# Kernel optimization log

Hardware: AMD Instinct MI355X
Metric: run time of the kernel (lower is better)

## Reference

```python
import jax, jax.numpy as jnp
import numpy as np
from jax.scipy.special import gammaln

# dims
S, B, T, N = 8, 128, 256, 128      # samples, trials, time bins, neurons
L, Hh, Hd, Hl = 64, 128, 64, 128   # latent, backward-enc h, dynamics hidden, local-enc hidden


def kl_diag(m, P, mu, Q):
    # KL(N(m, diag P) || N(mu, diag Q)), summed over last dim
    return 0.5 * jnp.sum(jnp.log(Q) - jnp.log(P) + (P + (m - mu) ** 2) / Q - 1.0, axis=-1)


def setup_inputs() -> dict:
    key = jax.random.key(0)
    ks = jax.random.split(key, 12)
    g = lambda i, shape, s=0.1: s * jax.random.normal(ks[i], shape, dtype=jnp.float32)
    y = jax.random.randint(ks[0], (B, T, N), 0, 5).astype(jnp.float32)  # spike counts
    return dict(
        y=y, n_samples=S,
        W_be=g(1, (N, Hh)), b_be=jnp.zeros((Hh,), jnp.float32),
        W_ic=g(2, (Hh, 2 * L)), b_ic=jnp.zeros((2 * L,), jnp.float32),
        W_le1=g(3, (Hh + L, Hl)), b_le1=jnp.zeros((Hl,), jnp.float32),
        W_le2=g(4, (Hl, 2 * L)), b_le2=jnp.zeros((2 * L,), jnp.float32),
        W_dyn1=g(5, (L, Hd)), b_dyn1=jnp.zeros((Hd,), jnp.float32),
        W_dyn2=g(6, (Hd, L)), b_dyn2=jnp.zeros((L,), jnp.float32),
        C=g(7, (L, N)), b_c=jnp.full((N,), -1.0, jnp.float32),
        log_Q=jnp.full((L,), -2.0, jnp.float32),
        m_0=jnp.zeros((L,), jnp.float32),
        log_Q_0=jnp.zeros((L,), jnp.float32),
        eps0=jax.random.normal(ks[8], (S, B, L), dtype=jnp.float32),
        eps=jax.random.normal(ks[9], (T - 1, S, B, L), dtype=jnp.float32),
    )


def reference(y, n_samples, W_be, b_be, W_ic, b_ic, W_le1, b_le1, W_le2, b_le2,
              W_dyn1, b_dyn1, W_dyn2, b_dyn2, C, b_c, log_Q, m_0, log_Q_0, eps0, eps):
    Q = jax.nn.softplus(log_Q)
    Q0 = jax.nn.softplus(log_Q_0)

    # backward encoder: per-step MLP y -> h  [B,T,Hh]
    h = jnp.tanh(y @ W_be + b_be)

    # t = 0: init_c_encoder on h[:,0]
    mp0 = h[:, 0] @ W_ic + b_ic
    m0e, P0 = mp0[..., :L], jax.nn.softplus(mp0[..., L:])
    z0 = m0e + jnp.sqrt(P0) * eps0                       # [S,B,L]
    kl0 = kl_diag(m0e, P0, m_0, Q0)                      # [B]

    def mean_fn(z):
        return jnp.tanh(z @ W_dyn1 + b_dyn1) @ W_dyn2 + b_dyn2

    def step(z_prev, xs):
        h_t, eps_t = xs                                  # [B,Hh], [S,B,L]
        inp = jnp.concatenate(
            [jnp.broadcast_to(h_t, (n_samples,) + h_t.shape), z_prev], axis=-1)
        mp = jnp.tanh(inp @ W_le1 + b_le1) @ W_le2 + b_le2
        m_t, P_t = mp[..., :L], jax.nn.softplus(mp[..., L:])
        z_t = m_t + jnp.sqrt(P_t) * eps_t                # [S,B,L]
        kl_t = kl_diag(m_t, P_t, mean_fn(z_prev), Q).mean(axis=0)  # [B]
        return z_t, (z_t, kl_t)

    h_rest = jnp.swapaxes(h[:, 1:], 0, 1)                # [T-1,B,Hh]
    _, (z_rest, kl_rest) = jax.lax.scan(step, z0, (h_rest, eps))

    z = jnp.concatenate([z0[:, :, None], jnp.moveaxis(z_rest, 0, 2)], axis=2)  # [S,B,T,L]
    kl = jnp.concatenate([kl0[:, None], kl_rest.T], axis=1)                    # [B,T]

    # Poisson log-likelihood, summed over neurons, averaged over samples
    log_rate = z @ C + b_c                               # [S,B,T,N]
    ell = jnp.sum(y * log_rate - jnp.exp(log_rate) - gammaln(y + 1.0), axis=-1).mean(axis=0)  # [B,T]

    loss = (kl - ell).sum(axis=-1).mean()
    m_stat = z.mean(axis=0)                              # [B,T,L]
    return loss, z, m_stat
```

## Files before the change

kernel.cpp:

```cpp
#include <hip/hip_runtime.h>

constexpr int S = 8, B = 128, T = 256, N = 128;
constexpr int L = 64, Hh = 128, Hd = 64, Hl = 128;
constexpr int BT = B * T;

#define DEVFN __device__ __forceinline__

typedef float    f32x4_t __attribute__((ext_vector_type(4)));
typedef _Float16 f16x8_t __attribute__((ext_vector_type(8)));
typedef _Float16 f16x4_t __attribute__((ext_vector_type(4)));

DEVFN float softplus_f(float x) {
    return (x > 0.f) ? (x + log1pf(expf(-x))) : log1pf(expf(x));
}
DEVFN float softplus_fast(float x) {
    return fmaxf(x, 0.f) + __logf(1.f + __expf(-fabsf(x)));
}
DEVFN float fast_tanh(float x) {
    float ex = __builtin_exp2f(x * 2.885390081777927f);
    return 1.f - 2.f / (ex + 1.f);
}
DEVFN float gaOf(float yv) {
    int yi = (int)yv;
    return (yi < 2) ? 0.f
         : ((yi == 2) ? 0.6931471805599453f
         : ((yi == 3) ? 1.791759469228055f : 3.1780538303479458f));
}

__global__ __launch_bounds__(256) void kA(
        const float* __restrict__ y,
        const float* __restrict__ W_be, const float* __restrict__ b_be,
        const float* __restrict__ W_le1, const float* __restrict__ b_le1,
        float* __restrict__ A, float* __restrict__ h0) {
    __shared__ alignas(16) _Float16 yS[32][136];
    __shared__ alignas(16) _Float16 hS[32][152];
    __shared__ alignas(16) float    st[32][136];
    __shared__ float bbeS[128];

    const int tid = threadIdx.x;
    const int w = tid >> 6, l = tid & 63;
    const int lo = l & 15, hi = l >> 4;
    const int bt0 = blockIdx.x * 32;

    if (tid < 128) bbeS[tid] = b_be[tid];

    {
        const float4* y4 = (const float4*)(y + (size_t)bt0 * 128);
        #pragma unroll
        for (int k = 0; k < 4; ++k) {
            int i = k * 256 + tid;
            float4 v = y4[i];
            int row = i >> 5, c4 = (i & 31) * 4;
            f16x4_t h4;
            h4[0] = (_Float16)v.x; h4[1] = (_Float16)v.y;
            h4[2] = (_Float16)v.z; h4[3] = (_Float16)v.w;
            *(f16x4_t*)&yS[row][c4] = h4;
        }
    }

    f16x8_t awb[2][4], awa[2][4];
    #pragma unroll
    for (int ct = 0; ct < 2; ++ct)
        #pragma unroll
        for (int kt = 0; kt < 4; ++kt) {
            f16x8_t f, g;
            #pragma unroll
            for (int e = 0; e < 8; ++e) {
                size_t off = (size_t)(kt * 32 + 8 * hi + e) * 128 + (32 * w + 16 * ct + lo);
                f[e] = (_Float16)W_be[off];
                g[e] = (_Float16)W_le1[off];
            }
            awb[ct][kt] = f; awa[ct][kt] = g;
        }
    const f32x4_t bl0 = *(const f32x4_t*)&b_le1[32 * w + 4 * hi];
    const f32x4_t bl1 = *(const f32x4_t*)&b_le1[32 * w + 16 + 4 * hi];
    __syncthreads();

    #pragma unroll
    for (int rt = 0; rt < 2; ++rt) {
        f32x4_t acc0 = {0.f,0.f,0.f,0.f}, acc1 = {0.f,0.f,0.f,0.f};
        #pragma unroll
        for (int kt = 0; kt < 4; ++kt) {
            const f16x8_t bf = *(const f16x8_t*)&yS[16 * rt + lo][kt * 32 + 8 * hi];
            acc0 = __builtin_amdgcn_mfma_f32_16x16x32_f16(awb[0][kt], bf, acc0, 0, 0, 0);
            acc1 = __builtin_amdgcn_mfma_f32_16x16x32_f16(awb[1][kt], bf, acc1, 0, 0, 0);
        }
        *(f32x4_t*)&st[16 * rt + lo][32 * w + 4 * hi]      = acc0;
        *(f32x4_t*)&st[16 * rt + lo][32 * w + 16 + 4 * hi] = acc1;
    }
    __syncthreads();

    {
        const int trow = tid >> 3, cb = (tid & 7) * 16;
        const bool isH0 = ((bt0 & 255) == 0) && (trow == 0);
        float* h0p = h0 + (size_t)(bt0 >> 8) * 128;
        #pragma unroll
        for (int j = 0; j < 16; ++j) {
            float hv = fast_tanh(st[trow][cb + j] + bbeS[cb + j]);
            hS[trow][cb + j] = (_Float16)hv;
            if (isH0) h0p[cb + j] = hv;
        }
    }
    __syncthreads();

    #pragma unroll
    for (int rt = 0; rt < 2; ++rt) {
        f32x4_t acc0 = {0.f,0.f,0.f,0.f}, acc1 = {0.f,0.f,0.f,0.f};
        #pragma unroll
        for (int kt = 0; kt < 4; ++kt) {
            const f16x8_t bf = *(const f16x8_t*)&hS[16 * rt + lo][kt * 32 + 8 * hi];
            acc0 = __builtin_amdgcn_mfma_f32_16x16x32_f16(awa[0][kt], bf, acc0, 0, 0, 0);
            acc1 = __builtin_amdgcn_mfma_f32_16x16x32_f16(awa[1][kt], bf, acc1, 0, 0, 0);
        }
        acc0 += bl0; acc1 += bl1;
        float* Ar = A + (size_t)(bt0 + 16 * rt + lo) * 128;
        *(f32x4_t*)&Ar[32 * w + 4 * hi]      = acc0;
        *(f32x4_t*)&Ar[32 * w + 16 + 4 * hi] = acc1;
    }
}

__global__ __launch_bounds__(256) void kC(
        const float* __restrict__ Aglob,
        const float* __restrict__ W_le1, const float* __restrict__ W_le2,
        const float* __restrict__ b_le2,
        const float* __restrict__ W_dyn1, const float* __restrict__ b_dyn1,
        const float* __restrict__ W_dyn2, const float* __restrict__ b_dyn2,
        const float* __restrict__ log_Q, const float* __restrict__ eps,
        const float* __restrict__ h0g, const float* __restrict__ W_ic,
        const float* __restrict__ b_ic, const float* __restrict__ m_0,
        const float* __restrict__ log_Q_0, const float* __restrict__ eps0,
        float* __restrict__ zout, float* __restrict__ kcl) {
    __shared__ alignas(16) _Float16 zSm[16][88];
    __shared__ alignas(16) _Float16 hidS[16][152];
    __shared__ alignas(16) _Float16 gS[16][88];
    __shared__ alignas(16) float stH[2][136];
    __shared__ alignas(16) float stG[2][72];
    __shared__ alignas(16) float stM[2][136];
    __shared__ alignas(16) float stMU[2][72];
    __shared__ float bmS[64], bpS[64], bmuS[64], bd1S[64], invQS[64];
    __shared__ float h0S[128], mpS[128];
    __shared__ float redK[4];

    const int tid = threadIdx.x;
    const int b = blockIdx.x >> 2, sq = blockIdx.x & 3, s0 = sq * 2;
    const int w = tid >> 6, l = tid & 63;
    const int lo = l & 15, hi = l >> 4;
    const bool prod = (lo < 2);

    {
        _Float16* p1 = &zSm[0][0];
        _Float16* p2 = &hidS[0][0];
        _Float16* p3 = &gS[0][0];
        for (int i = tid; i < 16 * 88; i += 256) { p1[i] = (_Float16)0.f; p3[i] = (_Float16)0.f; }
        for (int i = tid; i < 16 * 152; i += 256) p2[i] = (_Float16)0.f;
    }
    if (tid < 64) {
        bmS[tid]   = b_le2[tid];
        bpS[tid]   = b_le2[64 + tid];
        bmuS[tid]  = b_dyn2[tid];
        bd1S[tid]  = b_dyn1[tid];
        invQS[tid] = 1.f / softplus_f(log_Q[tid]);
    }
    if (tid < 128) h0S[tid] = h0g[(size_t)b * 128 + tid];

    f16x8_t a1[2][2], a2[2][4], a3[2], a4[2];
    #pragma unroll
    for (int ct = 0; ct < 2; ++ct)
        #pragma unroll
        for (int kt = 0; kt < 2; ++kt) {
            f16x8_t f;
            #pragma unroll
            for (int e = 0; e < 8; ++e)
                f[e] = (_Float16)W_le1[(size_t)(128 + kt * 32 + 8 * hi + e) * 128 + (32 * w + 16 * ct + lo)];
            a1[ct][kt] = f;
        }
    #pragma unroll
    for (int ct = 0; ct < 2; ++ct) {
        const int col = (ct == 0 ? 16 * w : 64 + 16 * w) + lo;
        #pragma unroll
        for (int kt = 0; kt < 4; ++kt) {
            f16x8_t f;
            #pragma unroll
            for (int e = 0; e < 8; ++e)
                f[e] = (_Float16)W_le2[(size_t)(kt * 32 + 8 * hi + e) * 128 + col];
            a2[ct][kt] = f;
        }
    }
    #pragma unroll
    for (int kt = 0; kt < 2; ++kt) {
        f16x8_t f, g;
        #pragma unroll
        for (int e = 0; e < 8; ++e) {
            f[e] = (_Float16)W_dyn1[(size_t)(kt * 32 + 8 * hi + e) * 64 + (16 * w + lo)];
            g[e] = (_Float16)W_dyn2[(size_t)(kt * 32 + 8 * hi + e) * 64 + (16 * w + lo)];
        }
        a3[kt] = f; a4[kt] = g;
    }

    const int ha = l >> 5, hc = 32 * w + (l & 31);
    const int ga2 = (l >> 4) & 1, gc = 16 * w + (l & 15);
    const int es = ga2, ec = gc;
    const float* ap = Aglob + ((size_t)b * T + 1) * 128 + hc;
    const float* ep = eps + (((size_t)(s0 + es)) * B + b) * 64 + ec;
    float*       zp = zout + ((((size_t)(s0 + es)) * B + b) * T + 1) * 64 + ec;

    float klAcc = 0.f;

    __syncthreads();

    if (tid < 128) {
        float acc = b_ic[tid];
        #pragma unroll 8
        for (int k = 0; k < 128; ++k) acc += h0S[k] * W_ic[(size_t)k * 128 + tid];
        mpS[tid] = acc;
    }
    __syncthreads();

    if (l < 32) {
        float m0v = mpS[ec];
        float P0  = softplus_f(mpS[64 + ec]);
        float e0  = eps0[(((size_t)(s0 + es)) * B + b) * 64 + ec];
        float z0  = m0v + sqrtf(P0) * e0;
        zout[((((size_t)(s0 + es)) * B + b) * T + 0) * 64 + ec] = z0;
        zSm[es][ec] = (_Float16)z0;
        if (sq == 0 && es == 0) {
            float Q0 = softplus_f(log_Q_0[ec]);
            float d0 = m0v - m_0[ec];
            klAcc += 8.f * (logf(Q0) - logf(P0) + (P0 + d0 * d0) / Q0 - 1.f);
        }
    }
    __syncthreads();

    float aN = *ap;
    float eN = 0.f;
    if (l < 32) eN = *ep;

    for (int t = 1; t < T; ++t) {
        const float aC = aN, eC = eN;

        if (t < T - 1) {
            ap += 128; aN = *ap;
            if (l < 32) { ep += (size_t)S * B * 64; eN = *ep; }
        }

        const f16x8_t bz0 = *(const f16x8_t*)&zSm[lo][8 * hi];
        const f16x8_t bz1 = *(const f16x8_t*)&zSm[lo][32 + 8 * hi];

        f32x4_t acc1a = {0.f,0.f,0.f,0.f}, acc1b = {0.f,0.f,0.f,0.f}, acc3 = {0.f,0.f,0.f,0.f};
        acc1a = __builtin_amdgcn_mfma_f32_16x16x32_f16(a1[0][0], bz0, acc1a, 0, 0, 0);
        acc1b = __builtin_amdgcn_mfma_f32_16x16x32_f16(a1[1][0], bz0, acc1b, 0, 0, 0);
        acc3  = __builtin_amdgcn_mfma_f32_16x16x32_f16(a3[0],    bz0, acc3,  0, 0, 0);
        acc1a = __builtin_amdgcn_mfma_f32_16x16x32_f16(a1[0][1], bz1, acc1a, 0, 0, 0);
        acc1b = __builtin_amdgcn_mfma_f32_16x16x32_f16(a1[1][1], bz1, acc1b, 0, 0, 0);
        acc3  = __builtin_amdgcn_mfma_f32_16x16x32_f16(a3[1],    bz1, acc3,  0, 0, 0);

        if (prod) {
            *(f32x4_t*)&stH[lo][32 * w + 4 * hi]      = acc1a;
            *(f32x4_t*)&stH[lo][32 * w + 16 + 4 * hi] = acc1b;
            *(f32x4_t*)&stG[lo][16 * w + 4 * hi]      = acc3;
        }
        asm volatile("" ::: "memory");

        hidS[ha][hc] = (_Float16)fast_tanh(stH[ha][hc] + aC);
        if (l < 32)
            gS[ga2][gc] = (_Float16)fast_tanh(stG[ga2][gc] + bd1S[gc]);
        __syncthreads();

        const f16x8_t bh0 = *(const f16x8_t*)&hidS[lo][ 0 + 8 * hi];
        const f16x8_t bh1 = *(const f16x8_t*)&hidS[lo][32 + 8 * hi];
        const f16x8_t bh2 = *(const f16x8_t*)&hidS[lo][64 + 8 * hi];
        const f16x8_t bh3 = *(const f16x8_t*)&hidS[lo][96 + 8 * hi];
        const f16x8_t bg0 = *(const f16x8_t*)&gS[lo][8 * hi];
        const f16x8_t bg1 = *(const f16x8_t*)&gS[lo][32 + 8 * hi];

        f32x4_t accm = {0.f,0.f,0.f,0.f}, accp = {0.f,0.f,0.f,0.f}, acc4 = {0.f,0.f,0.f,0.f};
        accm = __builtin_amdgcn_mfma_f32_16x16x32_f16(a2[0][0], bh0, accm, 0, 0, 0);
        accp = __builtin_amdgcn_mfma_f32_16x16x32_f16(a2[1][0], bh0, accp, 0, 0, 0);
        acc4 = __builtin_amdgcn_mfma_f32_16x16x32_f16(a4[0],    bg0, acc4, 0, 0, 0);
        accm = __builtin_amdgcn_mfma_f32_16x16x32_f16(a2[0][1], bh1, accm, 0, 0, 0);
        accp = __builtin_amdgcn_mfma_f32_16x16x32_f16(a2[1][1], bh1, accp, 0, 0, 0);
        acc4 = __builtin_amdgcn_mfma_f32_16x16x32_f16(a4[1],    bg1, acc4, 0, 0, 0);
        accm = __builtin_amdgcn_mfma_f32_16x16x32_f16(a2[0][2], bh2, accm, 0, 0, 0);
        accp = __builtin_amdgcn_mfma_f32_16x16x32_f16(a2[1][2], bh2, accp, 0, 0, 0);
        accm = __builtin_amdgcn_mfma_f32_16x16x32_f16(a2[0][3], bh3, accm, 0, 0, 0);
        accp = __builtin_amdgcn_mfma_f32_16x16x32_f16(a2[1][3], bh3, accp, 0, 0, 0);

        if (prod) {
            *(f32x4_t*)&stM[lo][16 * w + 4 * hi]       = accm;
            *(f32x4_t*)&stM[lo][64 + 16 * w + 4 * hi]  = accp;
            *(f32x4_t*)&stMU[lo][16 * w + 4 * hi]      = acc4;
        }
        asm volatile("" ::: "memory");

        if (l < 32) {
            float m  = stM[es][ec] + bmS[ec];
            float P  = softplus_fast(stM[es][64 + ec] + bpS[ec]);
            float mu = stMU[es][ec] + bmuS[ec];
            float iq = invQS[ec];
            float z  = m + sqrtf(P) * eC;
            *zp = z; zp += 64;
            zSm[es][ec] = (_Float16)z;
            float d = m - mu;
            klAcc += (P + d * d) * iq - __logf(P * iq) - 1.f;
        }
        __syncthreads();
    }

    float kv = klAcc;
    kv += __shfl_down(kv, 16);
    kv += __shfl_down(kv, 8);
    kv += __shfl_down(kv, 4);
    kv += __shfl_down(kv, 2);
    kv += __shfl_down(kv, 1);
    if (l == 0) redK[w] = kv;
    __syncthreads();
    if (tid == 0)
        kcl[blockIdx.x] = 0.0625f * (redK[0] + redK[1] + redK[2] + redK[3]);
}

__global__ __launch_bounds__(256) void kP2(
        const float* __restrict__ zin, const float* __restrict__ Cmat,
        const float* __restrict__ b_c, const float* __restrict__ yglob,
        float* __restrict__ m_stat, float* __restrict__ kel) {
    __shared__ alignas(16) _Float16 zP[16][72];
    __shared__ alignas(16) float yP[256];
    __shared__ float red4[4];

    const int tid = threadIdx.x;
    const int w = tid >> 6, l = tid & 63;
    const int lo = l & 15, hi = l >> 4;
    const int b = blockIdx.x >> 2, tq = blockIdx.x & 3;
    const int tbase = tq * 64;

    f16x8_t aC[2][2];
    #pragma unroll
    for (int ct = 0; ct < 2; ++ct)
        #pragma unroll
        for (int kt = 0; kt < 2; ++kt) {
            f16x8_t f;
            #pragma unroll
            for (int e = 0; e < 8; ++e)
                f[e] = (_Float16)Cmat[(size_t)(kt * 32 + 8 * hi + e) * 128 + (32 * w + 16 * ct + lo)];
            aC[ct][kt] = f;
        }
    f32x4_t bc[2];
    #pragma unroll
    for (int ct = 0; ct < 2; ++ct)
        #pragma unroll
        for (int r = 0; r < 4; ++r)
            bc[ct][r] = b_c[32 * w + 16 * ct + 4 * hi + r];

    float ellAcc = 0.f;

    for (int j = 0; j < 32; ++j) {
        const int t0 = tbase + 2 * j;
        __syncthreads();
        {
            int i = tid;
            int s = i >> 5, rem = i & 31;
            int tdx = rem >> 4, l4 = (rem & 15) * 4;
            f32x4_t v = *(const f32x4_t*)&zin[(((size_t)s * B + b) * T + t0 + tdx) * 64 + l4];
            f16x4_t h4;
            h4[0] = (_Float16)v[0]; h4[1] = (_Float16)v[1];
            h4[2] = (_Float16)v[2]; h4[3] = (_Float16)v[3];
            *(f16x4_t*)&zP[s * 2 + tdx][l4] = h4;
            yP[tid] = yglob[((size_t)b * T + t0) * 128 + tid];
        }
        __syncthreads();

        if (tid < 128) {
            int tdx = tid >> 6, ll = tid & 63;
            float acc = 0.f;
            #pragma unroll
            for (int s = 0; s < 8; ++s) acc += (float)zP[s * 2 + tdx][ll];
            m_stat[((size_t)b * T + t0 + tdx) * 64 + ll] = 0.125f * acc;
        }

        const f16x8_t bz0 = *(const f16x8_t*)&zP[lo][8 * hi];
        const f16x8_t bz1 = *(const f16x8_t*)&zP[lo][32 + 8 * hi];
        f32x4_t acc0 = {0.f,0.f,0.f,0.f}, acc1 = {0.f,0.f,0.f,0.f};
        acc0 = __builtin_amdgcn_mfma_f32_16x16x32_f16(aC[0][0], bz0, acc0, 0, 0, 0);
        acc1 = __builtin_amdgcn_mfma_f32_16x16x32_f16(aC[1][0], bz0, acc1, 0, 0, 0);
        acc0 = __builtin_amdgcn_mfma_f32_16x16x32_f16(aC[0][1], bz1, acc0, 0, 0, 0);
        acc1 = __builtin_amdgcn_mfma_f32_16x16x32_f16(aC[1][1], bz1, acc1, 0, 0, 0);

        {
            const int tdx = lo & 1;
            float te = 0.f;
            #pragma unroll
            for (int r = 0; r < 4; ++r) {
                int n0 = 32 * w + 4 * hi + r;
                float lr0 = acc0[r] + bc[0][r];
                float yv0 = yP[tdx * 128 + n0];
                te += yv0 * lr0 - __expf(lr0);
                int n1 = n0 + 16;
                float lr1 = acc1[r] + bc[1][r];
                float yv1 = yP[tdx * 128 + n1];
                te += yv1 * lr1 - __expf(lr1);
                if (lo < 2) te -= 8.f * (gaOf(yv0) + gaOf(yv1));
            }
            ellAcc += 0.125f * te;
        }
    }

    float ev = ellAcc;
    ev += __shfl_down(ev, 32);
    ev += __shfl_down(ev, 16);
    ev += __shfl_down(ev, 8);
    ev += __shfl_down(ev, 4);
    ev += __shfl_down(ev, 2);
    ev += __shfl_down(ev, 1);
    if (l == 0) red4[w] = ev;
    __syncthreads();
    if (tid == 0) kel[blockIdx.x] = red4[0] + red4[1] + red4[2] + red4[3];
}

__global__ __launch_bounds__(256) void kR(
        const float* __restrict__ kcl, const float* __restrict__ kel,
        float* __restrict__ out0) {
    __shared__ float red4[4];
    const int tid = threadIdx.x;
    float acc = 0.f;
    #pragma unroll
    for (int ii = 0; ii < 2; ii++) {
        int i = tid + ii * 256;
        acc += kcl[i] - kel[i];
    }
    #pragma unroll
    for (int off = 32; off; off >>= 1) acc += __shfl_down(acc, off);
    if ((tid & 63) == 0) red4[tid >> 6] = acc;
    __syncthreads();
    if (tid == 0) out0[0] = (red4[0] + red4[1] + red4[2] + red4[3]) * (1.0f / B);
}

extern "C" void kernel_launch(void* const* d_in, const int* in_sizes, int n_in,
                              void* d_out, int out_size, void* d_ws, size_t ws_size,
                              hipStream_t stream) {
    const float* y      = (const float*)d_in[0];
    const float* W_be   = (const float*)d_in[2];
    const float* b_be   = (const float*)d_in[3];
    const float* W_ic   = (const float*)d_in[4];
    const float* b_ic   = (const float*)d_in[5];
    const float* W_le1  = (const float*)d_in[6];
    const float* b_le1  = (const float*)d_in[7];
    const float* W_le2  = (const float*)d_in[8];
    const float* b_le2  = (const float*)d_in[9];
    const float* W_dyn1 = (const float*)d_in[10];
    const float* b_dyn1 = (const float*)d_in[11];
    const float* W_dyn2 = (const float*)d_in[12];
    const float* b_dyn2 = (const float*)d_in[13];
    const float* C      = (const float*)d_in[14];
    const float* b_c    = (const float*)d_in[15];
    const float* log_Q  = (const float*)d_in[16];
    const float* m_0    = (const float*)d_in[17];
    const float* log_Q_0= (const float*)d_in[18];
    const float* eps0   = (const float*)d_in[19];
    const float* eps    = (const float*)d_in[20];

    float* out = (float*)d_out;
    float* zo  = out + 1;
    float* ms  = out + 1 + (size_t)S * B * T * L;

    float* ws   = (float*)d_ws;
    float* kcl  = ws;
    float* kel  = kcl + 512;
    float* h0   = kel + 512;
    float* A    = h0 + (size_t)B * 128;

    kA<<<1024, 256, 0, stream>>>(y, W_be, b_be, W_le1, b_le1, A, h0);
    kC<<<512, 256, 0, stream>>>(A, W_le1, W_le2, b_le2, W_dyn1, b_dyn1,
                                W_dyn2, b_dyn2, log_Q, eps,
                                h0, W_ic, b_ic, m_0, log_Q_0, eps0,
                                zo, kcl);
    kP2<<<512, 256, 0, stream>>>(zo, C, b_c, y, ms, kel);
    kR<<<1, 256, 0, stream>>>(kcl, kel, out);
}
```

Before: 342.3 us.

## Interleave two independent sample chains per block in recurrent kernel

The recurrent kernel now processes four samples per block as two independent chains (X and Y) in double-buffered shared memory, staggered by half a step. Phase B of one chain runs alongside phase A of the other between barriers, so the number of barriers per sample step is halved and the latency of the dependent MFMA chains is hidden. The grid shrinks from 512 to 256 blocks and the reduction kernel is adjusted to match. The cost is fewer blocks for the GPU's CUs and more shared memory and registers per block.

```diff
diff --git a/kernel.cpp b/kernel.cpp
--- a/kernel.cpp
+++ b/kernel.cpp
@@ -130,29 +130,29 @@
         const float* __restrict__ b_ic, const float* __restrict__ m_0,
         const float* __restrict__ log_Q_0, const float* __restrict__ eps0,
         float* __restrict__ zout, float* __restrict__ kcl) {
-    __shared__ alignas(16) _Float16 zSm[16][88];
-    __shared__ alignas(16) _Float16 hidS[16][152];
-    __shared__ alignas(16) _Float16 gS[16][88];
-    __shared__ alignas(16) float stH[2][136];
-    __shared__ alignas(16) float stG[2][72];
-    __shared__ alignas(16) float stM[2][136];
-    __shared__ alignas(16) float stMU[2][72];
+    __shared__ alignas(16) _Float16 zSm[2][16][88];
+    __shared__ alignas(16) _Float16 hidS[2][16][152];
+    __shared__ alignas(16) _Float16 gS[2][16][88];
+    __shared__ alignas(16) float stH[2][16][136];
+    __shared__ alignas(16) float stG[2][16][72];
+    __shared__ alignas(16) float stM[2][16][136];
+    __shared__ alignas(16) float stMU[2][16][72];
     __shared__ float bmS[64], bpS[64], bmuS[64], bd1S[64], invQS[64];
     __shared__ float h0S[128], mpS[128];
     __shared__ float redK[4];
 
     const int tid = threadIdx.x;
-    const int b = blockIdx.x >> 2, sq = blockIdx.x & 3, s0 = sq * 2;
+    const int b = blockIdx.x >> 1, qq = blockIdx.x & 1;
+    const int s0X = 4 * qq, s0Y = 4 * qq + 2;
     const int w = tid >> 6, l = tid & 63;
     const int lo = l & 15, hi = l >> 4;
-    const bool prod = (lo < 2);
 
     {
-        _Float16* p1 = &zSm[0][0];
-        _Float16* p2 = &hidS[0][0];
-        _Float16* p3 = &gS[0][0];
-        for (int i = tid; i < 16 * 88; i += 256) { p1[i] = (_Float16)0.f; p3[i] = (_Float16)0.f; }
-        for (int i = tid; i < 16 * 152; i += 256) p2[i] = (_Float16)0.f;
+        _Float16* p1 = &zSm[0][0][0];
+        _Float16* p2 = &hidS[0][0][0];
+        _Float16* p3 = &gS[0][0][0];
+        for (int i = tid; i < 2 * 16 * 88; i += 256) { p1[i] = (_Float16)0.f; p3[i] = (_Float16)0.f; }
+        for (int i = tid; i < 2 * 16 * 152; i += 256) p2[i] = (_Float16)0.f;
     }
     if (tid < 64) {
         bmS[tid]   = b_le2[tid];
@@ -200,11 +200,68 @@
     const int ha = l >> 5, hc = 32 * w + (l & 31);
     const int ga2 = (l >> 4) & 1, gc = 16 * w + (l & 15);
     const int es = ga2, ec = gc;
-    const float* ap = Aglob + ((size_t)b * T + 1) * 128 + hc;
-    const float* ep = eps + (((size_t)(s0 + es)) * B + b) * 64 + ec;
-    float*       zp = zout + ((((size_t)(s0 + es)) * B + b) * T + 1) * 64 + ec;
-
-    float klAcc = 0.f;
+
+    const float* apX = Aglob + ((size_t)b * T + 2) * 128 + hc;
+    const float* apY = Aglob + ((size_t)b * T + 1) * 128 + hc;
+    const float* epX = eps + (((size_t)(s0X + es)) * B + b) * 64 + ec;
+    const float* epY = eps + (((size_t)(s0Y + es)) * B + b) * 64 + ec;
+    float* zpX = zout + ((((size_t)(s0X + es)) * B + b) * T + 1) * 64 + ec;
+    float* zpY = zout + ((((size_t)(s0Y + es)) * B + b) * T + 1) * 64 + ec;
+
+    float klAccX = 0.f, klAccY = 0.f;
+
+    auto PH_A = [&](int c, float aC) {
+        const f16x8_t bz0 = *(const f16x8_t*)&zSm[c][lo][8 * hi];
+        const f16x8_t bz1 = *(const f16x8_t*)&zSm[c][lo][32 + 8 * hi];
+        f32x4_t x1a = {0.f,0.f,0.f,0.f}, x1b = {0.f,0.f,0.f,0.f}, x3 = {0.f,0.f,0.f,0.f};
+        x1a = __builtin_amdgcn_mfma_f32_16x16x32_f16(a1[0][0], bz0, x1a, 0, 0, 0);
+        x1b = __builtin_amdgcn_mfma_f32_16x16x32_f16(a1[1][0], bz0, x1b, 0, 0, 0);
+        x3  = __builtin_amdgcn_mfma_f32_16x16x32_f16(a3[0],    bz0, x3,  0, 0, 0);
+        x1a = __builtin_amdgcn_mfma_f32_16x16x32_f16(a1[0][1], bz1, x1a, 0, 0, 0);
+        x1b = __builtin_amdgcn_mfma_f32_16x16x32_f16(a1[1][1], bz1, x1b, 0, 0, 0);
+        x3  = __builtin_amdgcn_mfma_f32_16x16x32_f16(a3[1],    bz1, x3,  0, 0, 0);
+        *(f32x4_t*)&stH[c][lo][32 * w + 4 * hi]      = x1a;
+        *(f32x4_t*)&stH[c][lo][32 * w + 16 + 4 * hi] = x1b;
+        *(f32x4_t*)&stG[c][lo][16 * w + 4 * hi]      = x3;
+        asm volatile("" ::: "memory");
+        hidS[c][ha][hc] = (_Float16)fast_tanh(stH[c][ha][hc] + aC);
+        if (l < 32)
+            gS[c][ga2][gc] = (_Float16)fast_tanh(stG[c][ga2][gc] + bd1S[gc]);
+    };
+    auto PH_B = [&](int c, float eC, float*& zp, float& klAcc) {
+        const f16x8_t bh0 = *(const f16x8_t*)&hidS[c][lo][ 0 + 8 * hi];
+        const f16x8_t bh1 = *(const f16x8_t*)&hidS[c][lo][32 + 8 * hi];
+        const f16x8_t bh2 = *(const f16x8_t*)&hidS[c][lo][64 + 8 * hi];
+        const f16x8_t bh3 = *(const f16x8_t*)&hidS[c][lo][96 + 8 * hi];
+        const f16x8_t bg0 = *(const f16x8_t*)&gS[c][lo][8 * hi];
+        const f16x8_t bg1 = *(const f16x8_t*)&gS[c][lo][32 + 8 * hi];
+        f32x4_t xm = {0.f,0.f,0.f,0.f}, xp = {0.f,0.f,0.f,0.f}, x4 = {0.f,0.f,0.f,0.f};
+        xm = __builtin_amdgcn_mfma_f32_16x16x32_f16(a2[0][0], bh0, xm, 0, 0, 0);
+        xp = __builtin_amdgcn_mfma_f32_16x16x32_f16(a2[1][0], bh0, xp, 0, 0, 0);
+        x4 = __builtin_amdgcn_mfma_f32_16x16x32_f16(a4[0],    bg0, x4, 0, 0, 0);
+        xm = __builtin_amdgcn_mfma_f32_16x16x32_f16(a2[0][1], bh1, xm, 0, 0, 0);
+        xp = __builtin_amdgcn_mfma_f32_16x16x32_f16(a2[1][1], bh1, xp, 0, 0, 0);
+        x4 = __builtin_amdgcn_mfma_f32_16x16x32_f16(a4[1],    bg1, x4, 0, 0, 0);
+        xm = __builtin_amdgcn_mfma_f32_16x16x32_f16(a2[0][2], bh2, xm, 0, 0, 0);
+        xp = __builtin_amdgcn_mfma_f32_16x16x32_f16(a2[1][2], bh2, xp, 0, 0, 0);
+        xm = __builtin_amdgcn_mfma_f32_16x16x32_f16(a2[0][3], bh3, xm, 0, 0, 0);
+        xp = __builtin_amdgcn_mfma_f32_16x16x32_f16(a2[1][3], bh3, xp, 0, 0, 0);
+        *(f32x4_t*)&stM[c][lo][16 * w + 4 * hi]       = xm;
+        *(f32x4_t*)&stM[c][lo][64 + 16 * w + 4 * hi]  = xp;
+        *(f32x4_t*)&stMU[c][lo][16 * w + 4 * hi]      = x4;
+        asm volatile("" ::: "memory");
+        if (l < 32) {
+            float m  = stM[c][es][ec] + bmS[ec];
+            float P  = softplus_fast(stM[c][es][64 + ec] + bpS[ec]);
+            float mu = stMU[c][es][ec] + bmuS[ec];
+            float iq = invQS[ec];
+            float z  = m + sqrtf(P) * eC;
+            *zp = z; zp += 64;
+            zSm[c][es][ec] = (_Float16)z;
+            float d = m - mu;
+            klAcc += (P + d * d) * iq - __logf(P * iq) - 1.f;
+        }
+    };
 
     __syncthreads();
 
@@ -219,94 +276,54 @@
     if (l < 32) {
         float m0v = mpS[ec];
         float P0  = softplus_f(mpS[64 + ec]);
-        float e0  = eps0[(((size_t)(s0 + es)) * B + b) * 64 + ec];
-        float z0  = m0v + sqrtf(P0) * e0;
-        zout[((((size_t)(s0 + es)) * B + b) * T + 0) * 64 + ec] = z0;
-        zSm[es][ec] = (_Float16)z0;
-        if (sq == 0 && es == 0) {
+        float sp0 = sqrtf(P0);
+        float e0x = eps0[(((size_t)(s0X + es)) * B + b) * 64 + ec];
+        float z0x = m0v + sp0 * e0x;
+        zout[((((size_t)(s0X + es)) * B + b) * T + 0) * 64 + ec] = z0x;
+        zSm[0][es][ec] = (_Float16)z0x;
+        float e0y = eps0[(((size_t)(s0Y + es)) * B + b) * 64 + ec];
+        float z0y = m0v + sp0 * e0y;
+        zout[((((size_t)(s0Y + es)) * B + b) * T + 0) * 64 + ec] = z0y;
+        zSm[1][es][ec] = (_Float16)z0y;
+        if (qq == 0 && es == 0) {
             float Q0 = softplus_f(log_Q_0[ec]);
             float d0 = m0v - m_0[ec];
-            klAcc += 8.f * (logf(Q0) - logf(P0) + (P0 + d0 * d0) / Q0 - 1.f);
-        }
-    }
-    __syncthreads();
-
-    float aN = *ap;
-    float eN = 0.f;
-    if (l < 32) eN = *ep;
+            klAccX += 8.f * (logf(Q0) - logf(P0) + (P0 + d0 * d0) / Q0 - 1.f);
+        }
+    }
+    __syncthreads();
+
+    {
+        float aX1 = Aglob[((size_t)b * T + 1) * 128 + hc];
+        PH_A(0, aX1);
+    }
+    float aNX = *apX;
+    float aNY = *apY;
+    float eNX = 0.f, eNY = 0.f;
+    if (l < 32) { eNX = *epX; eNY = *epY; }
+    __syncthreads();
 
     for (int t = 1; t < T; ++t) {
-        const float aC = aN, eC = eN;
-
+        const float aCX = aNX, aCY = aNY, eCX = eNX, eCY = eNY;
+        if (t < T - 2) { apX += 128; aNX = *apX; }
         if (t < T - 1) {
-            ap += 128; aN = *ap;
-            if (l < 32) { ep += (size_t)S * B * 64; eN = *ep; }
-        }
-
-        const f16x8_t bz0 = *(const f16x8_t*)&zSm[lo][8 * hi];
-        const f16x8_t bz1 = *(const f16x8_t*)&zSm[lo][32 + 8 * hi];
-
-        f32x4_t acc1a = {0.f,0.f,0.f,0.f}, acc1b = {0.f,0.f,0.f,0.f}, acc3 = {0.f,0.f,0.f,0.f};
-        acc1a = __builtin_amdgcn_mfma_f32_16x16x32_f16(a1[0][0], bz0, acc1a, 0, 0, 0);
-        acc1b = __builtin_amdgcn_mfma_f32_16x16x32_f16(a1[1][0], bz0, acc1b, 0, 0, 0);
-        acc3  = __builtin_amdgcn_mfma_f32_16x16x32_f16(a3[0],    bz0, acc3,  0, 0, 0);
-        acc1a = __builtin_amdgcn_mfma_f32_16x16x32_f16(a1[0][1], bz1, acc1a, 0, 0, 0);
-        acc1b = __builtin_amdgcn_mfma_f32_16x16x32_f16(a1[1][1], bz1, acc1b, 0, 0, 0);
-        acc3  = __builtin_amdgcn_mfma_f32_16x16x32_f16(a3[1],    bz1, acc3,  0, 0, 0);
-
-        if (prod) {
-            *(f32x4_t*)&stH[lo][32 * w + 4 * hi]      = acc1a;
-            *(f32x4_t*)&stH[lo][32 * w + 16 + 4 * hi] = acc1b;
-            *(f32x4_t*)&stG[lo][16 * w + 4 * hi]      = acc3;
-        }
-        asm volatile("" ::: "memory");
-
-        hidS[ha][hc] = (_Float16)fast_tanh(stH[ha][hc] + aC);
-        if (l < 32)
-            gS[ga2][gc] = (_Float16)fast_tanh(stG[ga2][gc] + bd1S[gc]);
+            apY += 128; aNY = *apY;
+            if (l < 32) {
+                epX += (size_t)S * B * 64; eNX = *epX;
+                epY += (size_t)S * B * 64; eNY = *epY;
+            }
+        }
+
+        PH_B(0, eCX, zpX, klAccX);
+        PH_A(1, aCY);
         __syncthreads();
 
-        const f16x8_t bh0 = *(const f16x8_t*)&hidS[lo][ 0 + 8 * hi];
-        const f16x8_t bh1 = *(const f16x8_t*)&hidS[lo][32 + 8 * hi];
-        const f16x8_t bh2 = *(const f16x8_t*)&hidS[lo][64 + 8 * hi];
-        const f16x8_t bh3 = *(const f16x8_t*)&hidS[lo][96 + 8 * hi];
-        const f16x8_t bg0 = *(const f16x8_t*)&gS[lo][8 * hi];
-        const f16x8_t bg1 = *(const f16x8_t*)&gS[lo][32 + 8 * hi];
-
-        f32x4_t accm = {0.f,0.f,0.f,0.f}, accp = {0.f,0.f,0.f,0.f}, acc4 = {0.f,0.f,0.f,0.f};
-        accm = __builtin_amdgcn_mfma_f32_16x16x32_f16(a2[0][0], bh0, accm, 0, 0, 0);
-        accp = __builtin_amdgcn_mfma_f32_16x16x32_f16(a2[1][0], bh0, accp, 0, 0, 0);
-        acc4 = __builtin_amdgcn_mfma_f32_16x16x32_f16(a4[0],    bg0, acc4, 0, 0, 0);
-        accm = __builtin_amdgcn_mfma_f32_16x16x32_f16(a2[0][1], bh1, accm, 0, 0, 0);
-        accp = __builtin_amdgcn_mfma_f32_16x16x32_f16(a2[1][1], bh1, accp, 0, 0, 0);
-        acc4 = __builtin_amdgcn_mfma_f32_16x16x32_f16(a4[1],    bg1, acc4, 0, 0, 0);
-        accm = __builtin_amdgcn_mfma_f32_16x16x32_f16(a2[0][2], bh2, accm, 0, 0, 0);
-        accp = __builtin_amdgcn_mfma_f32_16x16x32_f16(a2[1][2], bh2, accp, 0, 0, 0);
-        accm = __builtin_amdgcn_mfma_f32_16x16x32_f16(a2[0][3], bh3, accm, 0, 0, 0);
-        accp = __builtin_amdgcn_mfma_f32_16x16x32_f16(a2[1][3], bh3, accp, 0, 0, 0);
-
-        if (prod) {
-            *(f32x4_t*)&stM[lo][16 * w + 4 * hi]       = accm;
-            *(f32x4_t*)&stM[lo][64 + 16 * w + 4 * hi]  = accp;
-            *(f32x4_t*)&stMU[lo][16 * w + 4 * hi]      = acc4;
-        }
-        asm volatile("" ::: "memory");
-
-        if (l < 32) {
-            float m  = stM[es][ec] + bmS[ec];
-            float P  = softplus_fast(stM[es][64 + ec] + bpS[ec]);
-            float mu = stMU[es][ec] + bmuS[ec];
-            float iq = invQS[ec];
-            float z  = m + sqrtf(P) * eC;
-            *zp = z; zp += 64;
-            zSm[es][ec] = (_Float16)z;
-            float d = m - mu;
-            klAcc += (P + d * d) * iq - __logf(P * iq) - 1.f;
-        }
+        if (t < T - 1) PH_A(0, aCX);
+        PH_B(1, eCY, zpY, klAccY);
         __syncthreads();
     }
 
-    float kv = klAcc;
+    float kv = klAccX + klAccY;
     kv += __shfl_down(kv, 16);
     kv += __shfl_down(kv, 8);
     kv += __shfl_down(kv, 4);
@@ -420,12 +437,7 @@
         float* __restrict__ out0) {
     __shared__ float red4[4];
     const int tid = threadIdx.x;
-    float acc = 0.f;
-    #pragma unroll
-    for (int ii = 0; ii < 2; ii++) {
-        int i = tid + ii * 256;
-        acc += kcl[i] - kel[i];
-    }
+    float acc = kcl[tid] - kel[tid] - kel[tid + 256];
     #pragma unroll
     for (int off = 32; off; off >>= 1) acc += __shfl_down(acc, off);
     if ((tid & 63) == 0) red4[tid >> 6] = acc;
@@ -463,12 +475,12 @@
 
     float* ws   = (float*)d_ws;
     float* kcl  = ws;
-    float* kel  = kcl + 512;
+    float* kel  = kcl + 256;
     float* h0   = kel + 512;
     float* A    = h0 + (size_t)B * 128;
 
     kA<<<1024, 256, 0, stream>>>(y, W_be, b_be, W_le1, b_le1, A, h0);
-    kC<<<512, 256, 0, stream>>>(A, W_le1, W_le2, b_le2, W_dyn1, b_dyn1,
+    kC<<<256, 256, 0, stream>>>(A, W_le1, W_le2, b_le2, W_dyn1, b_dyn1,
                                 W_dyn2, b_dyn2, log_Q, eps,
                                 h0, W_ic, b_ic, m_0, log_Q_0, eps0,
                                 zo, kcl);
```

Measured after the change: 523.9 us. +53.1%, slower.
